# Kernel tuning notes

Measured on AMD Instinct MI355X. Metric: run time of the kernel, lower is better.

## Reference

```python
import jax, jax.numpy as jnp
import numpy as np

HID, H, KV, D = 2048, 16, 4, 128
ROPE_THETA = 10000.0
GATE_NORM = 16.0


def _rope_cos_sin(n, d, dtype=jnp.float32):
    inv_freq = 1.0 / (ROPE_THETA ** (jnp.arange(0, d, 2, dtype=jnp.float32) / d))
    freqs = jnp.arange(n, dtype=jnp.float32)[:, None] * inv_freq[None, :]  # (n, d/2)
    cos = jnp.cos(freqs).astype(dtype)[None, :, None, :]  # (1, n, 1, d/2)
    sin = jnp.sin(freqs).astype(dtype)[None, :, None, :]
    return cos, sin


def _apply_rotary(x, cos, sin):
    # x: (b, n, h, d); rotate-half (NeoX) convention over full head dim
    x1, x2 = jnp.split(x, 2, axis=-1)
    return jnp.concatenate([x1 * cos - x2 * sin, x2 * cos + x1 * sin], axis=-1)


def setup_inputs() -> dict:
    key = jax.random.key(0)
    k1, k2, k3, k4, k5 = jax.random.split(key, 5)
    s = 0.02  # realistic init scale for weights
    return {
        "hidden_states": jax.random.normal(k1, (1, 2048, HID), dtype=jnp.float32),
        "Wq": jax.random.normal(k2, (HID, H * D), dtype=jnp.float32) * s,
        "Wk": jax.random.normal(k3, (HID, KV * D), dtype=jnp.float32) * s,
        "Wv": jax.random.normal(k4, (HID, KV * D), dtype=jnp.float32) * s,
        "Wo": jax.random.normal(k5, (H * D, HID), dtype=jnp.float32) * s,
    }


def _forward(hidden_states, Wq, Wk, Wv, Wo):
    b, n, _ = hidden_states.shape
    groups = H // KV

    q = hidden_states @ Wq            # (b, n, H*D)
    k = hidden_states @ Wk            # (b, n, KV*D)
    v = hidden_states @ Wv            # (b, n, KV*D)
    # pool_g: AdaptiveAvgPool1d(KV*D) on a length-(KV*D) last dim == identity
    g = k

    q = q.reshape(b, n, H, D)
    k = k.reshape(b, n, KV, D)
    v = v.reshape(b, n, KV, D)
    g = g.reshape(b, n, KV, D)

    # GQA repeat to H heads
    k = jnp.repeat(k, groups, axis=2)
    v = jnp.repeat(v, groups, axis=2)
    g = jnp.repeat(g, groups, axis=2)

    sq, sk, sv = q, k, v  # raw (pre-softmax) tensors for the attention branch

    # GLA branch inputs: softmax'd q/k, log-sigmoid gates
    qs = jax.nn.softmax(q.astype(jnp.float32), axis=-1)
    ks = jax.nn.softmax(k.astype(jnp.float32), axis=-1)
    gl = jax.nn.log_sigmoid(g.astype(jnp.float32)) / GATE_NORM

    # rotary on raw q/k (seqlen_offset = 0)
    cos, sin = _rope_cos_sin(n, D)
    sq = _apply_rotary(sq, cos, sin)
    sk = _apply_rotary(sk, cos, sin)

    # --- gated linear attention recurrence (chunk_gla math, scale=1) ---
    def step(S, inp):
        q_t, k_t, v_t, g_t = inp  # each (b, H, D)
        S = S * jnp.exp(g_t)[..., None] + k_t[..., None] * v_t[..., None, :]
        o_t = jnp.einsum('bhk,bhkv->bhv', q_t, S)
        return S, o_t

    xs = tuple(jnp.moveaxis(a, 1, 0) for a in (qs, ks, v, gl))  # (n, b, H, D)
    S0 = jnp.zeros((b, H, D, D), dtype=jnp.float32)
    _, o_gla = jax.lax.scan(step, S0, xs)
    o_gla = jnp.moveaxis(o_gla, 0, 1)  # (b, n, H, D)

    # --- causal softmax attention (flash_attn_func, full window) ---
    scale = D ** -0.5
    scores = jnp.einsum('bqhd,bkhd->bhqk', sq, sk) * scale
    causal = jnp.tril(jnp.ones((n, n), dtype=bool))
    scores = jnp.where(causal[None, None], scores, jnp.finfo(scores.dtype).min)
    attn = jax.nn.softmax(scores, axis=-1)
    y = jnp.einsum('bhqk,bkhd->bqhd', attn, sv)

    o = 0.5 * y + 0.5 * o_gla
    o = o.reshape(b, n, H * D).astype(hidden_states.dtype)
    return o @ Wo


def reference(hidden_states, Wq, Wk, Wv, Wo):
    return _forward(hidden_states, Wq, Wk, Wv, Wo)
```

## Files before the change

kernel.cpp:

```cpp
#include <hip/hip_runtime.h>
#include <hip/hip_bf16.h>

typedef __bf16 bf16x8 __attribute__((ext_vector_type(8)));
typedef float f32x4 __attribute__((ext_vector_type(4)));
typedef float f32x16 __attribute__((ext_vector_type(16)));
typedef unsigned u32x4 __attribute__((ext_vector_type(4)));

#define MFMA16(a,b,c) __builtin_amdgcn_mfma_f32_16x16x32_bf16((a),(b),(c),0,0,0)
#define MFMA32(a,b,c) __builtin_amdgcn_mfma_f32_32x32x16_bf16((a),(b),(c),0,0,0)

__device__ __forceinline__ float bf2f(const __hip_bfloat16 h){ return __bfloat162float(h); }
__device__ __forceinline__ __hip_bfloat16 f2bf(float f){ return __float2bfloat16(f); }

__device__ __forceinline__ unsigned pk2(float a, float b){
  unsigned lo = __builtin_bit_cast(unsigned short, __float2bfloat16(a));
  unsigned hi = __builtin_bit_cast(unsigned short, __float2bfloat16(b));
  return lo | (hi << 16);
}
__device__ __forceinline__ void pl32swap(unsigned &x, unsigned &y){
  asm volatile("v_permlane32_swap_b32 %0, %1" : "+v"(x), "+v"(y));
}
__device__ __forceinline__ void gload16(const void* g, void* l){
  __builtin_amdgcn_global_load_lds((const __attribute__((address_space(1))) unsigned int*)g,
                                   (__attribute__((address_space(3))) unsigned int*)l, 16, 0, 0);
}

__device__ __forceinline__ size_t pk_idx(int grp, int ntile, int t, int d){
  int t32 = t >> 5, ql = t & 31, i = d >> 4, kh = (d >> 3) & 1, j = d & 7;
  return ((size_t)(grp*ntile + t32)*8 + i)*512 + (kh*32 + ql)*8 + j;
}
__device__ __forceinline__ size_t ep_idx(int grp, int t, int d){
  int t16 = t >> 4, lr = t & 15, f = d >> 5, lg = (d >> 3) & 3, j = d & 7;
  return (((size_t)grp*128 + t16)*4 + f)*512 + (lg*16 + lr)*8 + j;
}

__global__ void k_rope_table(float* __restrict__ ct, float* __restrict__ st){
  int e = blockIdx.x*256 + threadIdx.x;
  if (e >= 2048*64) return;
  int t = e >> 6, d = e & 63;
  float inv = expf(-(float)d * 0.14391156831212787f);
  float ang = (float)t * inv;
  ct[e] = cosf(ang);
  st[e] = sinf(ang);
}

__global__ void k_cvt_bf16(const float* __restrict__ in, __hip_bfloat16* __restrict__ out, int n4){
  int i = blockIdx.x*256 + threadIdx.x;
  if (i >= n4) return;
  float4 v = reinterpret_cast<const float4*>(in)[i];
  ushort4 o;
  o.x = __builtin_bit_cast(unsigned short, f2bf(v.x));
  o.y = __builtin_bit_cast(unsigned short, f2bf(v.y));
  o.z = __builtin_bit_cast(unsigned short, f2bf(v.z));
  o.w = __builtin_bit_cast(unsigned short, f2bf(v.w));
  reinterpret_cast<ushort4*>(out)[i] = o;
}

__global__ __launch_bounds__(256) void k_transpose_bf16(const float* __restrict__ in,
                                                        __hip_bfloat16* __restrict__ out,
                                                        int R, int C, int ldIn){
  __shared__ float tile[64][65];
  int ct_ = blockIdx.x*64, rt = blockIdx.y*64;
  int tx = threadIdx.x & 63, ty = threadIdx.x >> 6;
  #pragma unroll
  for (int i=0;i<16;++i){ int lr = i*4 + ty; tile[lr][tx] = in[(size_t)(rt+lr)*ldIn + ct_+tx]; }
  __syncthreads();
  #pragma unroll
  for (int i=0;i<16;++i){ int lr = i*4 + ty; out[(size_t)(ct_+lr)*R + rt+tx] = f2bf(tile[tx][lr]); }
}

__global__ __launch_bounds__(256) void k_transpose_w(const float* __restrict__ Wq,
                                                     const float* __restrict__ Wk,
                                                     const float* __restrict__ Wv,
                                                     const float* __restrict__ Wo,
                                                     __hip_bfloat16* __restrict__ WqkvT,
                                                     __hip_bfloat16* __restrict__ WoT){
  __shared__ float tile[64][65];
  int id = blockIdx.x;
  const float* in; __hip_bfloat16* out; int C, bx, by;
  if (id < 1024)      { in=Wq; out=WqkvT;                         C=2048; bx=id&31;          by=id>>5; }
  else if (id < 1280) { int i=id-1024; in=Wk; out=WqkvT+(size_t)2048*2048; C=512; bx=i&7;    by=i>>3; }
  else if (id < 1536) { int i=id-1280; in=Wv; out=WqkvT+(size_t)2560*2048; C=512; bx=i&7;    by=i>>3; }
  else                { int i=id-1536; in=Wo; out=WoT;            C=2048; bx=i&31;           by=i>>5; }
  const int R = 2048;
  int ct_ = bx*64, rt = by*64;
  int tx = threadIdx.x & 63, ty = threadIdx.x >> 6;
  #pragma unroll
  for (int i=0;i<16;++i){ int lr = i*4 + ty; tile[lr][tx] = in[(size_t)(rt+lr)*C + ct_+tx]; }
  __syncthreads();
  #pragma unroll
  for (int i=0;i<16;++i){ int lr = i*4 + ty; out[(size_t)(ct_+lr)*R + rt+tx] = f2bf(tile[tx][lr]); }
}

__global__ __launch_bounds__(128) void k_gemm_lds2(const __hip_bfloat16* __restrict__ A,
                                                   const __hip_bfloat16* __restrict__ BT,
                                                   float* __restrict__ C, int M, int N, int K){
  __shared__ __hip_bfloat16 As[128*64];
  __shared__ __hip_bfloat16 Bs[64*64];
  int nwg = gridDim.x;
  int cpx = nwg >> 3;
  int wg  = blockIdx.x;
  int swz = (wg & 7)*cpx + (wg >> 3);
  int nbx = N >> 6;
  int bn = (swz % nbx)*64, bm = (swz / nbx)*128;
  int tid = threadIdx.x, w = tid >> 6, l = tid & 63, lr = l & 15, lg = l >> 4;
  int wr = w*64;
  int srow = tid >> 3;
  int scol = (tid & 7)*8;
  f32x4 z = {0.f,0.f,0.f,0.f};
  f32x4 acc[4][4];
  #pragma unroll
  for (int i=0;i<4;++i){
    #pragma unroll
    for (int j=0;j<4;++j) acc[i][j] = z;
  }
  for (int bk=0; bk<K; bk+=64){
    #pragma unroll
    for (int i=0;i<8;++i)
      gload16(&A[(size_t)(bm + i*16 + srow)*K + bk + scol], &As[i*1024 + tid*8]);
    #pragma unroll
    for (int i=0;i<4;++i)
      gload16(&BT[(size_t)(bn + i*16 + srow)*K + bk + scol], &Bs[i*1024 + tid*8]);
    __syncthreads();
    __builtin_amdgcn_s_setprio(1);
    #pragma unroll
    for (int kk=0; kk<2; ++kk){
      bf16x8 af[4], bfr[4];
      #pragma unroll
      for (int mi=0;mi<4;++mi) af[mi]  = *reinterpret_cast<const bf16x8*>(&As[(wr+mi*16+lr)*64 + kk*32 + lg*8]);
      #pragma unroll
      for (int ni=0;ni<4;++ni) bfr[ni] = *reinterpret_cast<const bf16x8*>(&Bs[(ni*16+lr)*64 + kk*32 + lg*8]);
      #pragma unroll
      for (int mi=0;mi<4;++mi){
        #pragma unroll
        for (int ni=0;ni<4;++ni)
          acc[mi][ni] = MFMA16(af[mi], bfr[ni], acc[mi][ni]);
      }
    }
    __builtin_amdgcn_s_setprio(0);
    __syncthreads();
  }
  #pragma unroll
  for (int mi=0;mi<4;++mi){
    #pragma unroll
    for (int ni=0;ni<4;++ni){
      #pragma unroll
      for (int r=0;r<4;++r)
        C[(size_t)(bm+wr+mi*16+lg*4+r)*N + (bn+ni*16+lr)] = acc[mi][ni][r];
    }
  }
}

__global__ __launch_bounds__(128) void k_gates(const float* __restrict__ qkv,
                                               float* __restrict__ bt_all,
                                               float* __restrict__ eC){
  int c = blockIdx.x, kv = blockIdx.y, k = threadIdx.x;
  float b = 0.f;
  #pragma unroll 8
  for (int t=0;t<64;++t){
    float x = qkv[(size_t)(c*64+t)*3072 + 2048 + kv*128 + k];
    float gl = (fminf(x,0.f) - log1pf(expf(-fabsf(x)))) * 0.09016844005f;
    b += gl;
    bt_all[(size_t)(c*64+t)*512 + kv*128 + k] = b;
  }
  eC[((size_t)kv*32 + c)*128 + k] = exp2f(b);
}

__global__ __launch_bounds__(256) void k_qkpost(const float* __restrict__ qkv, const float* __restrict__ ct,
                                                const float* __restrict__ st, const float* __restrict__ bt_all,
                                                __hip_bfloat16* __restrict__ qpk, __hip_bfloat16* __restrict__ qep,
                                                __hip_bfloat16* __restrict__ kpk, __hip_bfloat16* __restrict__ ke,
                                                __hip_bfloat16* __restrict__ kep){
  int bid = blockIdx.x;
  int i = threadIdx.x & 63;
  if (bid < 8192){
    int g = bid*4 + (threadIdx.x >> 6);
    int t = g >> 4, h = g & 15;
    size_t base = (size_t)t*3072 + h*128;
    float a = qkv[base + i], b = qkv[base + 64 + i];
    float mx = fmaxf(a,b);
    #pragma unroll
    for (int off=1; off<64; off<<=1) mx = fmaxf(mx, __shfl_xor(mx, off));
    float ea = expf(a-mx), eb = expf(b-mx);
    float sm = ea+eb;
    #pragma unroll
    for (int off=1; off<64; off<<=1) sm += __shfl_xor(sm, off);
    float r = 1.0f/sm;
    const float* bp = &bt_all[(size_t)t*512 + (h>>2)*128];
    qep[ep_idx(h, t, i)]    = f2bf(exp2f(bp[i])    * (ea*r));
    qep[ep_idx(h, t, 64+i)] = f2bf(exp2f(bp[64+i]) * (eb*r));
    const float scale = 0.12751745f;
    float co = ct[t*64+i], si = st[t*64+i];
    qpk[pk_idx(h, 64, t, i)]    = f2bf((a*co - b*si)*scale);
    qpk[pk_idx(h, 64, t, 64+i)] = f2bf((b*co + a*si)*scale);
  } else {
    int g = (bid-8192)*4 + (threadIdx.x >> 6);
    int t = g >> 2, kv = g & 3;
    size_t base = (size_t)t*3072 + 2048 + kv*128;
    float a = qkv[base + i], b = qkv[base + 64 + i];
    float mx = fmaxf(a,b);
    #pragma unroll
    for (int off=1; off<64; off<<=1) mx = fmaxf(mx, __shfl_xor(mx, off));
    float ea = expf(a-mx), eb = expf(b-mx);
    float sm = ea+eb;
    #pragma unroll
    for (int off=1; off<64; off<<=1) sm += __shfl_xor(sm, off);
    float r = 1.0f/sm;
    const float* bp = &bt_all[(size_t)t*512 + kv*128];
    float kea = exp2f(-bp[i])    * (ea*r);
    float keb = exp2f(-bp[64+i]) * (eb*r);
    size_t ob = ((size_t)t*4 + kv)*128;
    ke[ob+i]    = f2bf(kea);
    ke[ob+64+i] = f2bf(keb);
    kep[ep_idx(kv, t, i)]    = f2bf(kea);
    kep[ep_idx(kv, t, 64+i)] = f2bf(keb);
    float co = ct[t*64+i], si = st[t*64+i];
    kpk[pk_idx(kv, 64, t, i)]    = f2bf(a*co - b*si);
    kpk[pk_idx(kv, 64, t, 64+i)] = f2bf(b*co + a*si);
  }
}

__global__ __launch_bounds__(256) void k_vpack(const __hip_bfloat16* __restrict__ vt,
                                               __hip_bfloat16* __restrict__ vpk,
                                               __hip_bfloat16* __restrict__ vpk16){
  int s = blockIdx.x, kv = blockIdx.y;
  int tid = threadIdx.x, l = tid & 63;
  int dt = tid >> 6;
  #pragma unroll
  for (int kq=0; kq<4; ++kq){
    bf16x8 v = *reinterpret_cast<const bf16x8*>(&vt[((size_t)kv*128 + dt*32 + (l&31))*2048 + s*64 + kq*16 + (l>>5)*8]);
    *reinterpret_cast<bf16x8*>(&vpk[((((size_t)kv*32 + s)*4 + dt)*4 + kq)*512 + l*8]) = v;
  }
  #pragma unroll
  for (int idx=0; idx<4; ++idx){
    int oc = dt*2 + (idx>>1), f2 = idx&1;
    bf16x8 v = *reinterpret_cast<const bf16x8*>(&vt[((size_t)kv*128 + oc*16 + (l&15))*2048 + s*64 + f2*32 + (l>>4)*8]);
    *reinterpret_cast<bf16x8*>(&vpk16[((((size_t)kv*32 + s)*8 + oc)*2 + f2)*512 + l*8]) = v;
  }
}

__global__ __launch_bounds__(256) void k_ckv(const __hip_bfloat16* __restrict__ ke,
                                             const __hip_bfloat16* __restrict__ vt,
                                             float* __restrict__ ckv){
  __shared__ __hip_bfloat16 kt[128*72];
  int c = blockIdx.x, kv = blockIdx.y;
  int tid = threadIdx.x, w = tid>>6, l = tid&63, lr=l&15, lg=l>>4;
  int wr = (w>>1)*64, wc = (w&1)*64;
  #pragma unroll
  for (int r=0;r<4;++r){
    int idx = r*256 + tid;
    int t  = idx >> 4;
    int k0 = (idx & 15)*8;
    bf16x8 v = *reinterpret_cast<const bf16x8*>(&ke[((size_t)(c*64+t)*4 + kv)*128 + k0]);
    #pragma unroll
    for (int j=0;j<8;++j) kt[(k0+j)*72 + t] = __builtin_bit_cast(__hip_bfloat16, (unsigned short)__builtin_bit_cast(unsigned short, v[j]));
  }
  __syncthreads();
  f32x4 z = {0.f,0.f,0.f,0.f};
  f32x4 acc[4][4];
  #pragma unroll
  for (int i=0;i<4;++i){
    #pragma unroll
    for (int j=0;j<4;++j) acc[i][j]=z;
  }
  size_t sb = (size_t)kv*32 + c;
  #pragma unroll
  for (int kf2=0;kf2<2;++kf2){
    bf16x8 af[4], bfr[4];
    #pragma unroll
    for (int mi=0;mi<4;++mi)
      af[mi] = *reinterpret_cast<const bf16x8*>(&kt[(wr+mi*16+lr)*72 + kf2*32 + lg*8]);
    #pragma unroll
    for (int ni=0;ni<4;++ni)
      bfr[ni] = *reinterpret_cast<const bf16x8*>(&vt[((size_t)kv*128 + wc+ni*16+lr)*2048 + c*64 + kf2*32 + lg*8]);
    #pragma unroll
    for (int mi=0;mi<4;++mi){
      #pragma unroll
      for (int ni=0;ni<4;++ni)
        acc[mi][ni] = MFMA16(af[mi], bfr[ni], acc[mi][ni]);
    }
  }
  #pragma unroll
  for (int mi=0;mi<4;++mi){
    #pragma unroll
    for (int ni=0;ni<4;++ni){
      #pragma unroll
      for (int r=0;r<4;++r)
        ckv[(sb*128 + wr+mi*16+lg*4+r)*128 + wc+ni*16+lr] = acc[mi][ni][r];
    }
  }
}

__global__ __launch_bounds__(256) void k_scan(const float* __restrict__ ckv, const float* __restrict__ eC,
                                              __hip_bfloat16* __restrict__ Stp){
  __shared__ float lds[8*128];
  int kv = blockIdx.y, bx = blockIdx.x;
  int tid = threadIdx.x;
  int kloc = tid >> 5;
  int kd  = bx*8 + kloc;
  int vd  = (tid*4) & 127;
  int oc = tid >> 5, lr = (tid >> 1) & 15, jh = (tid & 1)*4;
  int f  = bx >> 2, lg = bx & 3;
  float s0=0.f,s1=0.f,s2=0.f,s3=0.f;
  size_t sb0 = (size_t)kv*32;
  float e = eC[sb0*128 + kd];
  float4 u = reinterpret_cast<const float4*>(&ckv[(sb0*128 + kd)*128 + vd])[0];
  for (int c=0;c<32;++c){
    size_t sb = sb0 + c;
    float e_n = 0.f; float4 u_n = {0.f,0.f,0.f,0.f};
    if (c < 31){
      e_n = eC[(sb+1)*128 + kd];
      u_n = reinterpret_cast<const float4*>(&ckv[((sb+1)*128 + kd)*128 + vd])[0];
    }
    float4 cur = {s0,s1,s2,s3};
    *reinterpret_cast<float4*>(&lds[kloc*128 + vd]) = cur;
    __syncthreads();
    unsigned w0 = pk2(lds[(jh+0)*128 + oc*16+lr], lds[(jh+1)*128 + oc*16+lr]);
    unsigned w1 = pk2(lds[(jh+2)*128 + oc*16+lr], lds[(jh+3)*128 + oc*16+lr]);
    unsigned* dst = reinterpret_cast<unsigned*>(&Stp[((sb*8+oc)*4+f)*512 + (lg*16+lr)*8 + jh]);
    dst[0]=w0; dst[1]=w1;
    __syncthreads();
    s0 = (s0 + u.x)*e; s1 = (s1 + u.y)*e; s2 = (s2 + u.z)*e; s3 = (s3 + u.w)*e;
    e = e_n; u = u_n;
  }
}

__global__ __launch_bounds__(256) void k_attn(const __hip_bfloat16* __restrict__ qpk,
                                              const __hip_bfloat16* __restrict__ kpk,
                                              const __hip_bfloat16* __restrict__ vpk,
                                              float* __restrict__ ocomb){
  __shared__ __hip_bfloat16 OW[4][32][138];
  __shared__ float mW[4][32], lW[4][32];
  int h = blockIdx.y, kvh = h >> 2;
  int tid = threadIdx.x, w = tid >> 6, l = tid & 63;
  int ql = l & 31, kh = l >> 5;

  #pragma unroll 1
  for (int half=0; half<2; ++half){
    int qt = half ? (63 - (int)blockIdx.x) : (int)blockIdx.x;
    int qbase = qt*32;
    int qg = qbase + ql;

    bf16x8 qf[8];
    #pragma unroll
    for (int i=0;i<8;++i)
      qf[i] = *reinterpret_cast<const bf16x8*>(&qpk[((size_t)(h*64 + qt)*8 + i)*512 + l*8]);

    f32x16 zz = {0.f,0.f,0.f,0.f,0.f,0.f,0.f,0.f,0.f,0.f,0.f,0.f,0.f,0.f,0.f,0.f};
    f32x16 of[4];
    #pragma unroll
    for (int dt=0;dt<4;++dt) of[dt] = zz;
    float m = -1e30f, ll = 0.f;

    int nstep = qt/2 + 1;
    for (int s=w; s<nstep; s+=4){
      int kb = s*64;
      bool last = (s == nstep-1);
      f32x16 s0 = zz, s1 = zz;
      #pragma unroll
      for (int i=0;i<8;++i){
        bf16x8 k0 = *reinterpret_cast<const bf16x8*>(&kpk[((size_t)(kvh*64 + 2*s)*8 + i)*512 + l*8]);
        s0 = MFMA32(k0, qf[i], s0);
      }
      #pragma unroll
      for (int i=0;i<8;++i){
        bf16x8 k1 = *reinterpret_cast<const bf16x8*>(&kpk[((size_t)(kvh*64 + 2*s+1)*8 + i)*512 + l*8]);
        s1 = MFMA32(k1, qf[i], s1);
      }
      if (last){
        #pragma unroll
        for (int r=0;r<16;++r){
          int kr = (r&3) + 8*(r>>2) + 4*kh;
          if (kb + kr > qg)      s0[r] = -1e30f;
          if (kb + 32 + kr > qg) s1[r] = -1e30f;
        }
      }
      float pmax = fmaxf(s0[0], s1[0]);
      #pragma unroll
      for (int r=1;r<16;++r) pmax = fmaxf(pmax, fmaxf(s0[r], s1[r]));
      pmax = fmaxf(pmax, __shfl_xor(pmax, 32));
      if (!__all(pmax <= m + 11.54f)){
        float nm = fmaxf(m, pmax);
        float ef = exp2f(m - nm);
        ll *= ef;
        #pragma unroll
        for (int dt=0;dt<4;++dt){
          #pragma unroll
          for (int r=0;r<16;++r) of[dt][r] *= ef;
        }
        m = nm;
      }
      float ps = 0.f;
      #pragma unroll
      for (int r=0;r<16;++r){ s0[r] = exp2f(s0[r]-m); ps += s0[r]; }
      #pragma unroll
      for (int r=0;r<16;++r){ s1[r] = exp2f(s1[r]-m); ps += s1[r]; }
      ps += __shfl_xor(ps, 32);
      ll += ps;
      unsigned pw[4][4];
      {
        unsigned a,b;
        a = pk2(s0[0],s0[1]);   b = pk2(s0[4],s0[5]);   pl32swap(a,b); pw[0][0]=a; pw[0][2]=b;
        a = pk2(s0[2],s0[3]);   b = pk2(s0[6],s0[7]);   pl32swap(a,b); pw[0][1]=a; pw[0][3]=b;
        a = pk2(s0[8],s0[9]);   b = pk2(s0[12],s0[13]); pl32swap(a,b); pw[1][0]=a; pw[1][2]=b;
        a = pk2(s0[10],s0[11]); b = pk2(s0[14],s0[15]); pl32swap(a,b); pw[1][1]=a; pw[1][3]=b;
        a = pk2(s1[0],s1[1]);   b = pk2(s1[4],s1[5]);   pl32swap(a,b); pw[2][0]=a; pw[2][2]=b;
        a = pk2(s1[2],s1[3]);   b = pk2(s1[6],s1[7]);   pl32swap(a,b); pw[2][1]=a; pw[2][3]=b;
        a = pk2(s1[8],s1[9]);   b = pk2(s1[12],s1[13]); pl32swap(a,b); pw[3][0]=a; pw[3][2]=b;
        a = pk2(s1[10],s1[11]); b = pk2(s1[14],s1[15]); pl32swap(a,b); pw[3][1]=a; pw[3][3]=b;
      }
      #pragma unroll
      for (int dt=0; dt<4; ++dt){
        #pragma unroll
        for (int kq=0; kq<4; ++kq){
          bf16x8 vf = *reinterpret_cast<const bf16x8*>(&vpk[((((size_t)kvh*32 + s)*4 + dt)*4 + kq)*512 + l*8]);
          u32x4 pu = {pw[kq][0], pw[kq][1], pw[kq][2], pw[kq][3]};
          bf16x8 pb = __builtin_bit_cast(bf16x8, pu);
          of[dt] = MFMA32(vf, pb, of[dt]);
        }
      }
    }
    if (kh == 0){ mW[w][ql] = m; lW[w][ql] = ll; }
    #pragma unroll
    for (int dt=0; dt<4; ++dt){
      #pragma unroll
      for (int rp=0; rp<4; ++rp){
        unsigned lo = pk2(of[dt][rp*4+0], of[dt][rp*4+1]);
        unsigned hi = pk2(of[dt][rp*4+2], of[dt][rp*4+3]);
        unsigned* dst = reinterpret_cast<unsigned*>(&OW[w][ql][dt*32 + 8*rp + 4*kh]);
        dst[0] = lo; dst[1] = hi;
      }
    }
    __syncthreads();
    int q = tid >> 3, db = (tid & 7)*16;
    float m0=mW[0][q], m1=mW[1][q], m2=mW[2][q], m3=mW[3][q];
    float ms = fmaxf(fmaxf(m0,m1), fmaxf(m2,m3));
    float fac[4] = {exp2f(m0-ms), exp2f(m1-ms), exp2f(m2-ms), exp2f(m3-ms)};
    float lt = fac[0]*lW[0][q] + fac[1]*lW[1][q] + fac[2]*lW[2][q] + fac[3]*lW[3][q];
    float acc[16];
    #pragma unroll
    for (int j=0;j<16;++j) acc[j] = 0.f;
    #pragma unroll
    for (int wv=0; wv<4; ++wv){
      const unsigned* src = reinterpret_cast<const unsigned*>(&OW[wv][q][db]);
      float fx = fac[wv];
      #pragma unroll
      for (int j=0;j<8;++j){
        unsigned u = src[j];
        acc[2*j]   += fx * __builtin_bit_cast(float, u << 16);
        acc[2*j+1] += fx * __builtin_bit_cast(float, u & 0xffff0000u);
      }
    }
    float inv = 0.5f / lt;
    float4 o0 = {acc[0]*inv, acc[1]*inv, acc[2]*inv, acc[3]*inv};
    float4 o1 = {acc[4]*inv, acc[5]*inv, acc[6]*inv, acc[7]*inv};
    float4 o2 = {acc[8]*inv, acc[9]*inv, acc[10]*inv, acc[11]*inv};
    float4 o3 = {acc[12]*inv, acc[13]*inv, acc[14]*inv, acc[15]*inv};
    float4* dst = reinterpret_cast<float4*>(&ocomb[(size_t)(qbase+q)*2048 + h*128 + db]);
    dst[0]=o0; dst[1]=o1; dst[2]=o2; dst[3]=o3;
    __syncthreads();
  }
}

__global__ __launch_bounds__(256) void k_gla_out(const __hip_bfloat16* __restrict__ qep,
                                                 const __hip_bfloat16* __restrict__ kep,
                                                 const __hip_bfloat16* __restrict__ vpk16,
                                                 const __hip_bfloat16* __restrict__ Stp,
                                                 const float* __restrict__ ocomb,
                                                 __hip_bfloat16* __restrict__ obf){
  __shared__ __hip_bfloat16 ldsp[4*16*72];
  int c = blockIdx.x, h = blockIdx.y, kvh = h >> 2;
  int tid = threadIdx.x, w = tid>>6, l = tid&63, lr = l&15, lg = l>>4;
  int t0 = c*64, r0 = w*16;
  __hip_bfloat16* myp = &ldsp[w*16*72];
  bf16x8 qef[4];
  #pragma unroll
  for (int f=0; f<4; ++f)
    qef[f] = *reinterpret_cast<const bf16x8*>(&qep[(((size_t)h*128 + c*4 + w)*4 + f)*512 + l*8]);
  f32x4 z = {0.f,0.f,0.f,0.f};
  f32x4 of[8];
  #pragma unroll
  for (int oc=0;oc<8;++oc) of[oc]=z;
  __builtin_amdgcn_s_setprio(1);
  #pragma unroll
  for (int oc=0; oc<8; ++oc){
    #pragma unroll
    for (int f=0; f<4; ++f){
      bf16x8 sfr = *reinterpret_cast<const bf16x8*>(&Stp[((((size_t)kvh*32 + c)*8 + oc)*4 + f)*512 + l*8]);
      of[oc] = MFMA16(qef[f], sfr, of[oc]);
    }
  }
  f32x4 sacc[4] = {z,z,z,z};
  #pragma unroll
  for (int cb=0; cb<4; ++cb){
    #pragma unroll
    for (int f=0; f<4; ++f){
      bf16x8 kf = *reinterpret_cast<const bf16x8*>(&kep[(((size_t)kvh*128 + c*4 + cb)*4 + f)*512 + l*8]);
      sacc[cb] = MFMA16(qef[f], kf, sacc[cb]);
    }
  }
  __builtin_amdgcn_s_setprio(0);
  #pragma unroll
  for (int cb=0; cb<4; ++cb){
    #pragma unroll
    for (int r=0;r<4;++r){
      int s_ = cb*16 + lr;
      int t_ = r0 + lg*4 + r;
      float v = (s_ <= t_) ? sacc[cb][r] : 0.f;
      myp[(lg*4 + r)*72 + cb*16 + lr] = f2bf(v);
    }
  }
  bf16x8 pf[2];
  #pragma unroll
  for (int kf2=0;kf2<2;++kf2)
    pf[kf2] = *reinterpret_cast<const bf16x8*>(&myp[lr*72 + kf2*32 + lg*8]);
  __builtin_amdgcn_s_setprio(1);
  #pragma unroll
  for (int oc=0; oc<8; ++oc){
    #pragma unroll
    for (int kf2=0;kf2<2;++kf2){
      bf16x8 vf = *reinterpret_cast<const bf16x8*>(&vpk16[((((size_t)kvh*32 + c)*8 + oc)*2 + kf2)*512 + l*8]);
      of[oc] = MFMA16(pf[kf2], vf, of[oc]);
    }
  }
  __builtin_amdgcn_s_setprio(0);
  #pragma unroll
  for (int oc=0;oc<8;++oc){
    #pragma unroll
    for (int r=0;r<4;++r){
      int row = t0 + r0 + lg*4 + r;
      int col = h*128 + oc*16 + lr;
      float prev = ocomb[(size_t)row*2048 + col];
      obf[(size_t)row*2048 + col] = f2bf(prev + 0.5f*of[oc][r]);
    }
  }
}

extern "C" void kernel_launch(void* const* d_in, const int* in_sizes, int n_in,
                              void* d_out, int out_size, void* d_ws, size_t ws_size,
                              hipStream_t stream) {
  const float* hs = (const float*)d_in[0];
  const float* Wq = (const float*)d_in[1];
  const float* Wk = (const float*)d_in[2];
  const float* Wv = (const float*)d_in[3];
  const float* Wo = (const float*)d_in[4];
  float* out = (float*)d_out;

  char* base = (char*)d_ws;
  size_t off = 0;
  auto alloc = [&](size_t bytes) -> void* {
    void* p = base + off;
    off = (off + bytes + 255) & ~(size_t)255;
    return p;
  };

  float*          ropeC  = (float*)alloc(2048*64*4);
  float*          ropeS  = (float*)alloc(2048*64*4);
  __hip_bfloat16* hsb    = (__hip_bfloat16*)alloc((size_t)4194304*2);
  __hip_bfloat16* WqkvT  = (__hip_bfloat16*)alloc((size_t)3072*2048*2);
  __hip_bfloat16* WoT    = (__hip_bfloat16*)alloc((size_t)4194304*2);
  float*          qkv    = (float*)alloc((size_t)2048*3072*4);
  __hip_bfloat16* qpk    = (__hip_bfloat16*)alloc((size_t)4194304*2);
  __hip_bfloat16* kpk    = (__hip_bfloat16*)alloc((size_t)1048576*2);
  __hip_bfloat16* vt     = (__hip_bfloat16*)alloc((size_t)1048576*2);
  __hip_bfloat16* vpk    = (__hip_bfloat16*)alloc((size_t)1048576*2);
  __hip_bfloat16* vpk16  = (__hip_bfloat16*)alloc((size_t)1048576*2);
  __hip_bfloat16* qep    = (__hip_bfloat16*)alloc((size_t)4194304*2);
  __hip_bfloat16* ke     = (__hip_bfloat16*)alloc((size_t)1048576*2);
  __hip_bfloat16* kep    = (__hip_bfloat16*)alloc((size_t)1048576*2);
  float*          bt_all = (float*)alloc((size_t)1048576*4);
  float*          eC     = (float*)alloc((size_t)4*32*128*4);
  float*          ckv    = (float*)alloc((size_t)4*32*128*128*4);
  __hip_bfloat16* Stp    = (__hip_bfloat16*)alloc((size_t)4*32*128*128*2);
  float*          ocomb  = qkv;
  __hip_bfloat16* obf    = hsb;

  if (off > ws_size) return;

  k_rope_table<<<512, 256, 0, stream>>>(ropeC, ropeS);
  k_cvt_bf16<<<4096, 256, 0, stream>>>(hs, hsb, 1048576);
  k_transpose_w<<<dim3(2560), 256, 0, stream>>>(Wq, Wk, Wv, Wo, WqkvT, WoT);

  k_gemm_lds2<<<dim3(768), 128, 0, stream>>>(hsb, WqkvT, qkv, 2048, 3072, 2048);

  k_gates<<<dim3(32,4), 128, 0, stream>>>(qkv, bt_all, eC);
  k_qkpost<<<dim3(10240), 256, 0, stream>>>(qkv, ropeC, ropeS, bt_all, qpk, qep, kpk, ke, kep);
  k_transpose_bf16<<<dim3(8,32), 256, 0, stream>>>(qkv + 2560, vt, 2048, 512, 3072);
  k_vpack<<<dim3(32,4), 256, 0, stream>>>(vt, vpk, vpk16);

  k_ckv<<<dim3(32,4), 256, 0, stream>>>(ke, vt, ckv);
  k_scan<<<dim3(16,4), 256, 0, stream>>>(ckv, eC, Stp);

  k_attn<<<dim3(32,16), 256, 0, stream>>>(qpk, kpk, vpk, ocomb);
  k_gla_out<<<dim3(32,16), 256, 0, stream>>>(qep, kep, vpk16, Stp, ocomb, obf);

  k_gemm_lds2<<<dim3(512), 128, 0, stream>>>(obf, WoT, out, 2048, 2048, 2048);
}
```

Baseline: 269.9 us.

## Fuse V transpose/pack into one kernel and split attention into one tile per block

Replaces the separate V transpose and V pack kernels with a single kernel that stages a 64x128 fp32 V tile in shared memory and emits vt, vpk and vpk16 directly, removing one launch and a global round trip. The attention kernel now processes one 32-row query tile per block on a 64x16 grid, instead of pairing a light and a heavy tile in a loop, doubling block count at the cost of less balanced per-block work. Q fragments are reloaded from global memory inside the key loop rather than held in registers, lowering register pressure at the cost of repeated loads.

```diff
diff --git a/kernel.cpp b/kernel.cpp
--- a/kernel.cpp
+++ b/kernel.cpp
@@ -11,6 +11,9 @@
 
 __device__ __forceinline__ float bf2f(const __hip_bfloat16 h){ return __bfloat162float(h); }
 __device__ __forceinline__ __hip_bfloat16 f2bf(float f){ return __float2bfloat16(f); }
+__device__ __forceinline__ __bf16 f2raw(float f){
+  return __builtin_bit_cast(__bf16, __builtin_bit_cast(unsigned short, __float2bfloat16(f)));
+}
 
 __device__ __forceinline__ unsigned pk2(float a, float b){
   unsigned lo = __builtin_bit_cast(unsigned short, __float2bfloat16(a));
@@ -54,19 +57,6 @@
   o.z = __builtin_bit_cast(unsigned short, f2bf(v.z));
   o.w = __builtin_bit_cast(unsigned short, f2bf(v.w));
   reinterpret_cast<ushort4*>(out)[i] = o;
-}
-
-__global__ __launch_bounds__(256) void k_transpose_bf16(const float* __restrict__ in,
-                                                        __hip_bfloat16* __restrict__ out,
-                                                        int R, int C, int ldIn){
-  __shared__ float tile[64][65];
-  int ct_ = blockIdx.x*64, rt = blockIdx.y*64;
-  int tx = threadIdx.x & 63, ty = threadIdx.x >> 6;
-  #pragma unroll
-  for (int i=0;i<16;++i){ int lr = i*4 + ty; tile[lr][tx] = in[(size_t)(rt+lr)*ldIn + ct_+tx]; }
-  __syncthreads();
-  #pragma unroll
-  for (int i=0;i<16;++i){ int lr = i*4 + ty; out[(size_t)(ct_+lr)*R + rt+tx] = f2bf(tile[tx][lr]); }
 }
 
 __global__ __launch_bounds__(256) void k_transpose_w(const float* __restrict__ Wq,
@@ -220,22 +210,49 @@
   }
 }
 
-__global__ __launch_bounds__(256) void k_vpack(const __hip_bfloat16* __restrict__ vt,
+__global__ __launch_bounds__(256) void k_vprep(const float* __restrict__ qkv,
+                                               __hip_bfloat16* __restrict__ vt,
                                                __hip_bfloat16* __restrict__ vpk,
                                                __hip_bfloat16* __restrict__ vpk16){
+  __shared__ float lds[64*132];
   int s = blockIdx.x, kv = blockIdx.y;
-  int tid = threadIdx.x, l = tid & 63;
-  int dt = tid >> 6;
-  #pragma unroll
-  for (int kq=0; kq<4; ++kq){
-    bf16x8 v = *reinterpret_cast<const bf16x8*>(&vt[((size_t)kv*128 + dt*32 + (l&31))*2048 + s*64 + kq*16 + (l>>5)*8]);
-    *reinterpret_cast<bf16x8*>(&vpk[((((size_t)kv*32 + s)*4 + dt)*4 + kq)*512 + l*8]) = v;
-  }
-  #pragma unroll
-  for (int idx=0; idx<4; ++idx){
-    int oc = dt*2 + (idx>>1), f2 = idx&1;
-    bf16x8 v = *reinterpret_cast<const bf16x8*>(&vt[((size_t)kv*128 + oc*16 + (l&15))*2048 + s*64 + f2*32 + (l>>4)*8]);
-    *reinterpret_cast<bf16x8*>(&vpk16[((((size_t)kv*32 + s)*8 + oc)*2 + f2)*512 + l*8]) = v;
+  int tid = threadIdx.x;
+  #pragma unroll
+  for (int it=0; it<8; ++it){
+    int i = it*256 + tid;
+    int t = i >> 5, dc = (i & 31)*4;
+    float4 v = *reinterpret_cast<const float4*>(&qkv[(size_t)(s*64+t)*3072 + 2560 + kv*128 + dc]);
+    *reinterpret_cast<float4*>(&lds[t*132 + dc]) = v;
+  }
+  __syncthreads();
+  #pragma unroll
+  for (int it=0; it<4; ++it){
+    int i = it*256 + tid;
+    int d = i >> 3, tg = (i & 7)*8;
+    bf16x8 o;
+    #pragma unroll
+    for (int j=0;j<8;++j) o[j] = f2raw(lds[(tg+j)*132 + d]);
+    *reinterpret_cast<bf16x8*>(&vt[((size_t)kv*128 + d)*2048 + s*64 + tg]) = o;
+  }
+  #pragma unroll
+  for (int it=0; it<4; ++it){
+    int j2 = it*256 + tid;
+    int dt = j2 >> 8, kq = (j2 >> 6) & 3, l = j2 & 63;
+    int ts = kq*16 + (l>>5)*8, ds = dt*32 + (l&31);
+    bf16x8 o;
+    #pragma unroll
+    for (int j=0;j<8;++j) o[j] = f2raw(lds[(ts+j)*132 + ds]);
+    *reinterpret_cast<bf16x8*>(&vpk[((((size_t)kv*32 + s)*4 + dt)*4 + kq)*512 + l*8]) = o;
+  }
+  #pragma unroll
+  for (int it=0; it<4; ++it){
+    int j3 = it*256 + tid;
+    int oc = j3 >> 7, f2 = (j3 >> 6) & 1, l = j3 & 63;
+    int ts = f2*32 + (l>>4)*8, ds = oc*16 + (l&15);
+    bf16x8 o;
+    #pragma unroll
+    for (int j=0;j<8;++j) o[j] = f2raw(lds[(ts+j)*132 + ds]);
+    *reinterpret_cast<bf16x8*>(&vpk16[((((size_t)kv*32 + s)*8 + oc)*2 + f2)*512 + l*8]) = o;
   }
 }
 
@@ -334,132 +351,123 @@
   int h = blockIdx.y, kvh = h >> 2;
   int tid = threadIdx.x, w = tid >> 6, l = tid & 63;
   int ql = l & 31, kh = l >> 5;
-
-  #pragma unroll 1
-  for (int half=0; half<2; ++half){
-    int qt = half ? (63 - (int)blockIdx.x) : (int)blockIdx.x;
-    int qbase = qt*32;
-    int qg = qbase + ql;
-
-    bf16x8 qf[8];
-    #pragma unroll
-    for (int i=0;i<8;++i)
-      qf[i] = *reinterpret_cast<const bf16x8*>(&qpk[((size_t)(h*64 + qt)*8 + i)*512 + l*8]);
-
-    f32x16 zz = {0.f,0.f,0.f,0.f,0.f,0.f,0.f,0.f,0.f,0.f,0.f,0.f,0.f,0.f,0.f,0.f};
-    f32x16 of[4];
-    #pragma unroll
-    for (int dt=0;dt<4;++dt) of[dt] = zz;
-    float m = -1e30f, ll = 0.f;
-
-    int nstep = qt/2 + 1;
-    for (int s=w; s<nstep; s+=4){
-      int kb = s*64;
-      bool last = (s == nstep-1);
-      f32x16 s0 = zz, s1 = zz;
-      #pragma unroll
-      for (int i=0;i<8;++i){
-        bf16x8 k0 = *reinterpret_cast<const bf16x8*>(&kpk[((size_t)(kvh*64 + 2*s)*8 + i)*512 + l*8]);
-        s0 = MFMA32(k0, qf[i], s0);
+  int qt = 63 - (int)blockIdx.x;
+  int qbase = qt*32;
+  int qg = qbase + ql;
+  const __hip_bfloat16* qb = qpk + ((size_t)(h*64 + qt)*8)*512 + l*8;
+
+  f32x16 zz = {0.f,0.f,0.f,0.f,0.f,0.f,0.f,0.f,0.f,0.f,0.f,0.f,0.f,0.f,0.f,0.f};
+  f32x16 of[4];
+  #pragma unroll
+  for (int dt=0;dt<4;++dt) of[dt] = zz;
+  float m = -1e30f, ll = 0.f;
+
+  int nstep = qt/2 + 1;
+  for (int s=w; s<nstep; s+=4){
+    int kb = s*64;
+    bool last = (s == nstep-1);
+    f32x16 s0 = zz, s1 = zz;
+    const __hip_bfloat16* qv = qb;
+    #pragma unroll
+    for (int i=0;i<8;++i){
+      asm volatile("" : "+v"(qv));
+      bf16x8 qf = *reinterpret_cast<const bf16x8*>(qv + (size_t)i*512);
+      bf16x8 k0 = *reinterpret_cast<const bf16x8*>(&kpk[((size_t)(kvh*64 + 2*s)*8 + i)*512 + l*8]);
+      s0 = MFMA32(k0, qf, s0);
+      bf16x8 k1 = *reinterpret_cast<const bf16x8*>(&kpk[((size_t)(kvh*64 + 2*s+1)*8 + i)*512 + l*8]);
+      s1 = MFMA32(k1, qf, s1);
+    }
+    if (last){
+      #pragma unroll
+      for (int r=0;r<16;++r){
+        int kr = (r&3) + 8*(r>>2) + 4*kh;
+        if (kb + kr > qg)      s0[r] = -1e30f;
+        if (kb + 32 + kr > qg) s1[r] = -1e30f;
       }
-      #pragma unroll
-      for (int i=0;i<8;++i){
-        bf16x8 k1 = *reinterpret_cast<const bf16x8*>(&kpk[((size_t)(kvh*64 + 2*s+1)*8 + i)*512 + l*8]);
-        s1 = MFMA32(k1, qf[i], s1);
+    }
+    float pmax = fmaxf(s0[0], s1[0]);
+    #pragma unroll
+    for (int r=1;r<16;++r) pmax = fmaxf(pmax, fmaxf(s0[r], s1[r]));
+    pmax = fmaxf(pmax, __shfl_xor(pmax, 32));
+    if (!__all(pmax <= m + 11.54f)){
+      float nm = fmaxf(m, pmax);
+      float ef = exp2f(m - nm);
+      ll *= ef;
+      #pragma unroll
+      for (int dt=0;dt<4;++dt){
+        #pragma unroll
+        for (int r=0;r<16;++r) of[dt][r] *= ef;
       }
-      if (last){
-        #pragma unroll
-        for (int r=0;r<16;++r){
-          int kr = (r&3) + 8*(r>>2) + 4*kh;
-          if (kb + kr > qg)      s0[r] = -1e30f;
-          if (kb + 32 + kr > qg) s1[r] = -1e30f;
-        }
+      m = nm;
+    }
+    float ps = 0.f;
+    #pragma unroll
+    for (int r=0;r<16;++r){ s0[r] = exp2f(s0[r]-m); ps += s0[r]; }
+    #pragma unroll
+    for (int r=0;r<16;++r){ s1[r] = exp2f(s1[r]-m); ps += s1[r]; }
+    ps += __shfl_xor(ps, 32);
+    ll += ps;
+    unsigned pw[4][4];
+    {
+      unsigned a,b;
+      a = pk2(s0[0],s0[1]);   b = pk2(s0[4],s0[5]);   pl32swap(a,b); pw[0][0]=a; pw[0][2]=b;
+      a = pk2(s0[2],s0[3]);   b = pk2(s0[6],s0[7]);   pl32swap(a,b); pw[0][1]=a; pw[0][3]=b;
+      a = pk2(s0[8],s0[9]);   b = pk2(s0[12],s0[13]); pl32swap(a,b); pw[1][0]=a; pw[1][2]=b;
+      a = pk2(s0[10],s0[11]); b = pk2(s0[14],s0[15]); pl32swap(a,b); pw[1][1]=a; pw[1][3]=b;
+      a = pk2(s1[0],s1[1]);   b = pk2(s1[4],s1[5]);   pl32swap(a,b); pw[2][0]=a; pw[2][2]=b;
+      a = pk2(s1[2],s1[3]);   b = pk2(s1[6],s1[7]);   pl32swap(a,b); pw[2][1]=a; pw[2][3]=b;
+      a = pk2(s1[8],s1[9]);   b = pk2(s1[12],s1[13]); pl32swap(a,b); pw[3][0]=a; pw[3][2]=b;
+      a = pk2(s1[10],s1[11]); b = pk2(s1[14],s1[15]); pl32swap(a,b); pw[3][1]=a; pw[3][3]=b;
+    }
+    #pragma unroll
+    for (int dt=0; dt<4; ++dt){
+      #pragma unroll
+      for (int kq=0; kq<4; ++kq){
+        bf16x8 vf = *reinterpret_cast<const bf16x8*>(&vpk[((((size_t)kvh*32 + s)*4 + dt)*4 + kq)*512 + l*8]);
+        u32x4 pu = {pw[kq][0], pw[kq][1], pw[kq][2], pw[kq][3]};
+        bf16x8 pb = __builtin_bit_cast(bf16x8, pu);
+        of[dt] = MFMA32(vf, pb, of[dt]);
       }
-      float pmax = fmaxf(s0[0], s1[0]);
-      #pragma unroll
-      for (int r=1;r<16;++r) pmax = fmaxf(pmax, fmaxf(s0[r], s1[r]));
-      pmax = fmaxf(pmax, __shfl_xor(pmax, 32));
-      if (!__all(pmax <= m + 11.54f)){
-        float nm = fmaxf(m, pmax);
-        float ef = exp2f(m - nm);
-        ll *= ef;
-        #pragma unroll
-        for (int dt=0;dt<4;++dt){
-          #pragma unroll
-          for (int r=0;r<16;++r) of[dt][r] *= ef;
-        }
-        m = nm;
-      }
-      float ps = 0.f;
-      #pragma unroll
-      for (int r=0;r<16;++r){ s0[r] = exp2f(s0[r]-m); ps += s0[r]; }
-      #pragma unroll
-      for (int r=0;r<16;++r){ s1[r] = exp2f(s1[r]-m); ps += s1[r]; }
-      ps += __shfl_xor(ps, 32);
-      ll += ps;
-      unsigned pw[4][4];
-      {
-        unsigned a,b;
-        a = pk2(s0[0],s0[1]);   b = pk2(s0[4],s0[5]);   pl32swap(a,b); pw[0][0]=a; pw[0][2]=b;
-        a = pk2(s0[2],s0[3]);   b = pk2(s0[6],s0[7]);   pl32swap(a,b); pw[0][1]=a; pw[0][3]=b;
-        a = pk2(s0[8],s0[9]);   b = pk2(s0[12],s0[13]); pl32swap(a,b); pw[1][0]=a; pw[1][2]=b;
-        a = pk2(s0[10],s0[11]); b = pk2(s0[14],s0[15]); pl32swap(a,b); pw[1][1]=a; pw[1][3]=b;
-        a = pk2(s1[0],s1[1]);   b = pk2(s1[4],s1[5]);   pl32swap(a,b); pw[2][0]=a; pw[2][2]=b;
-        a = pk2(s1[2],s1[3]);   b = pk2(s1[6],s1[7]);   pl32swap(a,b); pw[2][1]=a; pw[2][3]=b;
-        a = pk2(s1[8],s1[9]);   b = pk2(s1[12],s1[13]); pl32swap(a,b); pw[3][0]=a; pw[3][2]=b;
-        a = pk2(s1[10],s1[11]); b = pk2(s1[14],s1[15]); pl32swap(a,b); pw[3][1]=a; pw[3][3]=b;
-      }
-      #pragma unroll
-      for (int dt=0; dt<4; ++dt){
-        #pragma unroll
-        for (int kq=0; kq<4; ++kq){
-          bf16x8 vf = *reinterpret_cast<const bf16x8*>(&vpk[((((size_t)kvh*32 + s)*4 + dt)*4 + kq)*512 + l*8]);
-          u32x4 pu = {pw[kq][0], pw[kq][1], pw[kq][2], pw[kq][3]};
-          bf16x8 pb = __builtin_bit_cast(bf16x8, pu);
-          of[dt] = MFMA32(vf, pb, of[dt]);
-        }
-      }
-    }
-    if (kh == 0){ mW[w][ql] = m; lW[w][ql] = ll; }
-    #pragma unroll
-    for (int dt=0; dt<4; ++dt){
-      #pragma unroll
-      for (int rp=0; rp<4; ++rp){
-        unsigned lo = pk2(of[dt][rp*4+0], of[dt][rp*4+1]);
-        unsigned hi = pk2(of[dt][rp*4+2], of[dt][rp*4+3]);
-        unsigned* dst = reinterpret_cast<unsigned*>(&OW[w][ql][dt*32 + 8*rp + 4*kh]);
-        dst[0] = lo; dst[1] = hi;
-      }
-    }
-    __syncthreads();
-    int q = tid >> 3, db = (tid & 7)*16;
-    float m0=mW[0][q], m1=mW[1][q], m2=mW[2][q], m3=mW[3][q];
-    float ms = fmaxf(fmaxf(m0,m1), fmaxf(m2,m3));
-    float fac[4] = {exp2f(m0-ms), exp2f(m1-ms), exp2f(m2-ms), exp2f(m3-ms)};
-    float lt = fac[0]*lW[0][q] + fac[1]*lW[1][q] + fac[2]*lW[2][q] + fac[3]*lW[3][q];
-    float acc[16];
-    #pragma unroll
-    for (int j=0;j<16;++j) acc[j] = 0.f;
-    #pragma unroll
-    for (int wv=0; wv<4; ++wv){
-      const unsigned* src = reinterpret_cast<const unsigned*>(&OW[wv][q][db]);
-      float fx = fac[wv];
-      #pragma unroll
-      for (int j=0;j<8;++j){
-        unsigned u = src[j];
-        acc[2*j]   += fx * __builtin_bit_cast(float, u << 16);
-        acc[2*j+1] += fx * __builtin_bit_cast(float, u & 0xffff0000u);
-      }
-    }
-    float inv = 0.5f / lt;
-    float4 o0 = {acc[0]*inv, acc[1]*inv, acc[2]*inv, acc[3]*inv};
-    float4 o1 = {acc[4]*inv, acc[5]*inv, acc[6]*inv, acc[7]*inv};
-    float4 o2 = {acc[8]*inv, acc[9]*inv, acc[10]*inv, acc[11]*inv};
-    float4 o3 = {acc[12]*inv, acc[13]*inv, acc[14]*inv, acc[15]*inv};
-    float4* dst = reinterpret_cast<float4*>(&ocomb[(size_t)(qbase+q)*2048 + h*128 + db]);
-    dst[0]=o0; dst[1]=o1; dst[2]=o2; dst[3]=o3;
-    __syncthreads();
-  }
+    }
+  }
+  if (kh == 0){ mW[w][ql] = m; lW[w][ql] = ll; }
+  #pragma unroll
+  for (int dt=0; dt<4; ++dt){
+    #pragma unroll
+    for (int rp=0; rp<4; ++rp){
+      unsigned lo = pk2(of[dt][rp*4+0], of[dt][rp*4+1]);
+      unsigned hi = pk2(of[dt][rp*4+2], of[dt][rp*4+3]);
+      unsigned* dst = reinterpret_cast<unsigned*>(&OW[w][ql][dt*32 + 8*rp + 4*kh]);
+      dst[0] = lo; dst[1] = hi;
+    }
+  }
+  __syncthreads();
+  int q = tid >> 3, db = (tid & 7)*16;
+  float m0=mW[0][q], m1=mW[1][q], m2=mW[2][q], m3=mW[3][q];
+  float ms = fmaxf(fmaxf(m0,m1), fmaxf(m2,m3));
+  float fac[4] = {exp2f(m0-ms), exp2f(m1-ms), exp2f(m2-ms), exp2f(m3-ms)};
+  float lt = fac[0]*lW[0][q] + fac[1]*lW[1][q] + fac[2]*lW[2][q] + fac[3]*lW[3][q];
+  float acc[16];
+  #pragma unroll
+  for (int j=0;j<16;++j) acc[j] = 0.f;
+  #pragma unroll
+  for (int wv=0; wv<4; ++wv){
+    const unsigned* src = reinterpret_cast<const unsigned*>(&OW[wv][q][db]);
+    float fx = fac[wv];
+    #pragma unroll
+    for (int j=0;j<8;++j){
+      unsigned u = src[j];
+      acc[2*j]   += fx * __builtin_bit_cast(float, u << 16);
+      acc[2*j+1] += fx * __builtin_bit_cast(float, u & 0xffff0000u);
+    }
+  }
+  float inv = 0.5f / lt;
+  float4 o0 = {acc[0]*inv, acc[1]*inv, acc[2]*inv, acc[3]*inv};
+  float4 o1 = {acc[4]*inv, acc[5]*inv, acc[6]*inv, acc[7]*inv};
+  float4 o2 = {acc[8]*inv, acc[9]*inv, acc[10]*inv, acc[11]*inv};
+  float4 o3 = {acc[12]*inv, acc[13]*inv, acc[14]*inv, acc[15]*inv};
+  float4* dst = reinterpret_cast<float4*>(&ocomb[(size_t)(qbase+q)*2048 + h*128 + db]);
+  dst[0]=o0; dst[1]=o1; dst[2]=o2; dst[3]=o3;
 }
 
 __global__ __launch_bounds__(256) void k_gla_out(const __hip_bfloat16* __restrict__ qep,
@@ -585,13 +593,12 @@
 
   k_gates<<<dim3(32,4), 128, 0, stream>>>(qkv, bt_all, eC);
   k_qkpost<<<dim3(10240), 256, 0, stream>>>(qkv, ropeC, ropeS, bt_all, qpk, qep, kpk, ke, kep);
-  k_transpose_bf16<<<dim3(8,32), 256, 0, stream>>>(qkv + 2560, vt, 2048, 512, 3072);
-  k_vpack<<<dim3(32,4), 256, 0, stream>>>(vt, vpk, vpk16);
+  k_vprep<<<dim3(32,4), 256, 0, stream>>>(qkv, vt, vpk, vpk16);
 
   k_ckv<<<dim3(32,4), 256, 0, stream>>>(ke, vt, ckv);
   k_scan<<<dim3(16,4), 256, 0, stream>>>(ckv, eC, Stp);
 
-  k_attn<<<dim3(32,16), 256, 0, stream>>>(qpk, kpk, vpk, ocomb);
+  k_attn<<<dim3(64,16), 256, 0, stream>>>(qpk, kpk, vpk, ocomb);
   k_gla_out<<<dim3(32,16), 256, 0, stream>>>(qep, kep, vpk16, Stp, ocomb, obf);
 
   k_gemm_lds2<<<dim3(512), 128, 0, stream>>>(obf, WoT, out, 2048, 2048, 2048);
```

Result: slower. 281.3 us (+4.2%).
